# Kernel tuning notes

Hardware: AMD Instinct MI355X
Metric: run time of the kernel (lower is better)

The kernel has to match this reference:

```python
import jax, jax.numpy as jnp
import numpy as np

B, N, DIM, H = 8, 1024, 768, 12
D = DIM // H
SCALE = D ** -0.5
EPS = 1e-5


def setup_inputs() -> dict:
    key = jax.random.key(0)
    ks = jax.random.split(key, 6)
    s = 0.02
    return {
        "x": jax.random.normal(ks[0], (B, N, DIM), jnp.float32),
        "w_qv": jax.random.normal(ks[1], (2 * DIM, DIM), jnp.float32) * s,
        "ext_k": jax.random.normal(ks[2], (1, H, N, D), jnp.float32),
        "ext_bias": jax.random.normal(ks[3], (1, H, N, N), jnp.float32),
        "bn_gamma": jnp.ones((H,), jnp.float32),
        "bn_beta": jnp.zeros((H,), jnp.float32),
        "w_proj": jax.random.normal(ks[4], (DIM, DIM), jnp.float32) * s,
        "b_proj": jnp.zeros((DIM,), jnp.float32),
    }


def reference(x, w_qv, ext_k, ext_bias, bn_gamma, bn_beta, w_proj, b_proj):
    b, n, c = x.shape
    # qv projection (no bias), split into q and v
    qv = jnp.einsum('bnc,ec->bne', x, w_qv)  # [B,N,2C]
    q, v = jnp.split(qv, 2, axis=-1)
    # b n (h d) -> b h n d
    q = q.reshape(b, n, H, D).transpose(0, 2, 1, 3)
    v = v.reshape(b, n, H, D).transpose(0, 2, 1, 3)
    # scores: (q @ ext_k^T + bias) * scale  -> [B,H,N,N]
    attn = (jnp.einsum('bhnd,xhmd->bhnm', q, ext_k) + ext_bias) * SCALE
    # BatchNorm2d over heads (training-mode batch stats over B,N,N)
    mean = jnp.mean(attn, axis=(0, 2, 3), keepdims=True)
    var = jnp.mean(jnp.square(attn - mean), axis=(0, 2, 3), keepdims=True)
    attn = (attn - mean) * jax.lax.rsqrt(var + EPS)
    attn = attn * bn_gamma[None, :, None, None] + bn_beta[None, :, None, None]
    # softmax over keys, dropout p=0
    attn = jax.nn.softmax(attn, axis=-1)
    out = jnp.einsum('bhnm,bhmd->bhnd', attn, v)
    out = out.transpose(0, 2, 1, 3).reshape(b, n, c)  # b h n d -> b n (h d)
    return jnp.einsum('bnc,oc->bno', out, w_proj) + b_proj
```

## Files before the change

kernel.cpp:

```cpp
#include <hip/hip_runtime.h>
#include <cstdint>

#define B_    8
#define N_    1024
#define DIM_  768
#define H_    12
#define D_    64
#define SCALE_ 0.125f
#define GQ_   32
#define GK_   4

typedef unsigned short u16;
typedef short bf16x8 __attribute__((ext_vector_type(8)));
typedef float f32x4  __attribute__((ext_vector_type(4)));

__device__ __forceinline__ u16 f2b(float f) {
  union { float f; unsigned u; } v; v.f = f;
  unsigned r = v.u + 0x7FFFu + ((v.u >> 16) & 1u);
  return (u16)(r >> 16);
}
__device__ __forceinline__ float b2f(u16 h) {
  union { unsigned u; float f; } v; v.u = ((unsigned)h) << 16; return v.f;
}
__device__ __forceinline__ void gl2lds16(const void* g, void* l) {
  __builtin_amdgcn_global_load_lds(
      (const __attribute__((address_space(1))) void*)g,
      (__attribute__((address_space(3))) void*)l, 16, 0, 0);
}

__global__ __launch_bounds__(256) void cast_all(
    const float4* __restrict__ s0, u16* __restrict__ d0, int n0,
    const float4* __restrict__ s1, u16* __restrict__ d1, int n1,
    const float4* __restrict__ s2, u16* __restrict__ d2, int n2,
    const float4* __restrict__ s3, u16* __restrict__ d3, int n3)
{
  int i = blockIdx.x * 256 + threadIdx.x;
  const float4* s; u16* d; int off;
  if (i < n0)               { s = s0; d = d0; off = i; }
  else if (i < n0+n1)       { s = s1; d = d1; off = i - n0; }
  else if (i < n0+n1+n2)    { s = s2; d = d2; off = i - n0 - n1; }
  else if (i < n0+n1+n2+n3) { s = s3; d = d3; off = i - n0 - n1 - n2; }
  else return;
  float4 v = s[off];
  ushort4 o; o.x = f2b(v.x); o.y = f2b(v.y); o.z = f2b(v.z); o.w = f2b(v.w);
  *(ushort4*)(d + (size_t)off * 4) = o;
}

__global__ __launch_bounds__(256) void qv_gemm(
    const u16* __restrict__ A, const u16* __restrict__ W,
    u16* __restrict__ qo, u16* __restrict__ vo)
{
  __shared__ u16 As[128*32];
  __shared__ u16 Bs[128*32];
  const int tid = threadIdx.x, lane = tid & 63, wid = tid >> 6;
  const int m0 = blockIdx.y * 128, n0 = blockIdx.x * 128;
  const int wm = (wid >> 1) * 64, wn = (wid & 1) * 64;
  const int lr = lane & 15, lq = lane >> 4;
  f32x4 acc[4][4] = {};
  for (int k0 = 0; k0 < 768; k0 += 32) {
#pragma unroll
    for (int it = 0; it < 2; ++it) {
      int c = it * 256 + tid;
      int row = c >> 2, c8 = c & 3;
      gl2lds16(A + (size_t)(m0 + row) * 768 + k0 + c8 * 8, (char*)As + (it*256 + wid*64) * 16);
      gl2lds16(W + (size_t)(n0 + row) * 768 + k0 + c8 * 8, (char*)Bs + (it*256 + wid*64) * 16);
    }
    __syncthreads();
    bf16x8 af[4], bfr[4];
#pragma unroll
    for (int i = 0; i < 4; ++i) {
      af[i]  = *(const bf16x8*)&As[(wm + i*16 + lr) * 32 + lq * 8];
      bfr[i] = *(const bf16x8*)&Bs[(wn + i*16 + lr) * 32 + lq * 8];
    }
#pragma unroll
    for (int mi = 0; mi < 4; ++mi)
#pragma unroll
      for (int nj = 0; nj < 4; ++nj)
        acc[mi][nj] = __builtin_amdgcn_mfma_f32_16x16x32_bf16(af[mi], bfr[nj], acc[mi][nj], 0, 0, 0);
    __syncthreads();
  }
#pragma unroll
  for (int mi = 0; mi < 4; ++mi)
#pragma unroll
    for (int nj = 0; nj < 4; ++nj)
#pragma unroll
      for (int r = 0; r < 4; ++r) {
        int row = m0 + wm + mi*16 + lq*4 + r;
        int col = n0 + wn + nj*16 + lr;
        u16 bv = f2b(acc[mi][nj][r]);
        int b = row >> 10, n = row & 1023;
        if (col < 768) { int h = col >> 6, d = col & 63;
          qo[(((size_t)(b*12 + h)) << 16) + (n << 6) + d] = bv;
        } else { int e = col - 768; int h = e >> 6, d = e & 63;
          vo[(((size_t)(b*12 + h)) << 16) + (n << 6) + d] = bv;
        }
      }
}

__global__ __launch_bounds__(256) void transpose_v(
    const u16* __restrict__ v, u16* __restrict__ vt,
    const u16* __restrict__ kk, u16* __restrict__ ktT)
{
  __shared__ u16 t[64][65];
  int y = blockIdx.y, n0 = blockIdx.x * 64, tid = threadIdx.x;
  const u16* src; u16* dst;
  if (y < 96) { src = v  + (((size_t)y) << 16) + (size_t)n0 * 64;      dst = vt  + (((size_t)y) << 16) + n0; }
  else { int h = y - 96; src = kk + (((size_t)h) << 16) + (size_t)n0 * 64; dst = ktT + (((size_t)h) << 16) + n0; }
#pragma unroll
  for (int i = 0; i < 16; ++i) {
    int e = i*256 + tid; t[e >> 6][e & 63] = src[e];
  }
  __syncthreads();
#pragma unroll
  for (int i = 0; i < 16; ++i) {
    int e = i*256 + tid; int d = e >> 6, r = e & 63;
    dst[(size_t)d * 1024 + r] = t[r][d];
  }
}

__global__ __launch_bounds__(256) void qs_kernel(const u16* __restrict__ q, float* __restrict__ qs)
{
  int idx = blockIdx.x * 256 + threadIdx.x;
  int h = idx >> 16, rem = idx & 65535;
  float s = 0.f;
#pragma unroll
  for (int b = 0; b < 8; ++b) s += b2f(q[(((size_t)(b*12 + h)) << 16) + rem]);
  qs[idx] = s;
}

__global__ __launch_bounds__(256) void gram_kernel(
    const u16* __restrict__ src, float* __restrict__ gpart,
    int rows_per_block, int b_interleaved)
{
  __shared__ float t[64*68];
  const int h = blockIdx.y, r0 = blockIdx.x * rows_per_block, tid = threadIdx.x;
  const int rr = (tid >> 4) * 4;
  const int cc = (tid & 15) * 4;
  float a[4][4] = {{0.f}};
  for (int t0 = 0; t0 < rows_per_block; t0 += 64) {
#pragma unroll
    for (int i = 0; i < 4; ++i) {
      int e = i*256 + tid;
      int r = e >> 4, d4 = (e & 15) * 4;
      int gr = r0 + t0 + r;
      size_t addr;
      if (b_interleaved) { int b = gr >> 10, n = gr & 1023;
        addr = (((size_t)(b*12 + h)) << 16) + (n << 6) + d4; }
      else addr = (((size_t)h) << 16) + ((size_t)gr << 6) + d4;
      ushort4 u = *(const ushort4*)(src + addr);
      float4 f; f.x = b2f(u.x); f.y = b2f(u.y); f.z = b2f(u.z); f.w = b2f(u.w);
      *(float4*)&t[r*68 + d4] = f;
    }
    __syncthreads();
#pragma unroll 4
    for (int m = 0; m < 64; ++m) {
      float4 rv = *(const float4*)&t[m*68 + rr];
      float4 cv = *(const float4*)&t[m*68 + cc];
      a[0][0] += rv.x*cv.x; a[0][1] += rv.x*cv.y; a[0][2] += rv.x*cv.z; a[0][3] += rv.x*cv.w;
      a[1][0] += rv.y*cv.x; a[1][1] += rv.y*cv.y; a[1][2] += rv.y*cv.z; a[1][3] += rv.y*cv.w;
      a[2][0] += rv.z*cv.x; a[2][1] += rv.z*cv.y; a[2][2] += rv.z*cv.z; a[2][3] += rv.z*cv.w;
      a[3][0] += rv.w*cv.x; a[3][1] += rv.w*cv.y; a[3][2] += rv.w*cv.z; a[3][3] += rv.w*cv.w;
    }
    __syncthreads();
  }
  float* g = gpart + (((size_t)blockIdx.x) * 12 + h) * 4096;
#pragma unroll
  for (int i = 0; i < 4; ++i)
    *(float4*)&g[(rr + i)*64 + cc] = make_float4(a[i][0], a[i][1], a[i][2], a[i][3]);
}

__global__ __launch_bounds__(256) void bias_stats(
    const float* __restrict__ bias, const u16* __restrict__ ktT,
    const float* __restrict__ qs, float* __restrict__ acc)
{
  __shared__ float red[12];
  const int tid = threadIdx.x, lane = tid & 63, wid = tid >> 6;
  const int lr = lane & 15, lq = lane >> 4;
  const int h = blockIdx.y;
  const int nb = blockIdx.x & 15, mb = blockIdx.x >> 4;
  const int n0 = nb * 64 + wid * 16;
  const size_t brow = (((size_t)h) << 20) + ((size_t)(n0 + lr) << 10);
  const size_t kbase = ((size_t)h) << 16;
  f32x4 kb[4] = {};
  float sb = 0.f, sb2 = 0.f;
#pragma unroll
  for (int ms = 0; ms < 4; ++ms) {
    const int m0 = mb * 256 + ms * 64;
#pragma unroll
    for (int ks = 0; ks < 2; ++ks) {
      const int mc = m0 + ks * 32 + lq * 8;
      float4 b0 = *(const float4*)(bias + brow + mc);
      float4 b1 = *(const float4*)(bias + brow + mc + 4);
      sb  += b0.x + b0.y + b0.z + b0.w + b1.x + b1.y + b1.z + b1.w;
      sb2 += b0.x*b0.x + b0.y*b0.y + b0.z*b0.z + b0.w*b0.w
           + b1.x*b1.x + b1.y*b1.y + b1.z*b1.z + b1.w*b1.w;
      union { bf16x8 v; u16 u[8]; } af;
      af.u[0] = f2b(b0.x); af.u[1] = f2b(b0.y); af.u[2] = f2b(b0.z); af.u[3] = f2b(b0.w);
      af.u[4] = f2b(b1.x); af.u[5] = f2b(b1.y); af.u[6] = f2b(b1.z); af.u[7] = f2b(b1.w);
#pragma unroll
      for (int dj = 0; dj < 4; ++dj) {
        bf16x8 bfr = *(const bf16x8*)(ktT + kbase + (size_t)(dj*16 + lr) * 1024 + mc);
        kb[dj] = __builtin_amdgcn_mfma_f32_16x16x32_bf16(af.v, bfr, kb[dj], 0, 0, 0);
      }
    }
  }
  float cross = 0.f;
#pragma unroll
  for (int dj = 0; dj < 4; ++dj)
#pragma unroll
    for (int r = 0; r < 4; ++r)
      cross += kb[dj][r] *
               qs[kbase + ((size_t)(nb*64 + wid*16 + lq*4 + r) << 6) + dj*16 + lr];
#pragma unroll
  for (int s = 32; s; s >>= 1) {
    sb += __shfl_xor(sb, s); sb2 += __shfl_xor(sb2, s); cross += __shfl_xor(cross, s);
  }
  if (lane == 0) { red[wid] = sb; red[4 + wid] = sb2; red[8 + wid] = cross; }
  __syncthreads();
  if (tid == 0) {
    atomicAdd(acc + h,      red[0] + red[1] + red[2] + red[3]);
    atomicAdd(acc + 12 + h, red[4] + red[5] + red[6] + red[7]);
    atomicAdd(acc + 24 + h, red[8] + red[9] + red[10] + red[11]);
  }
}

__global__ __launch_bounds__(256) void sums_kernel(
    const float* __restrict__ qs, const u16* __restrict__ kb16,
    float* __restrict__ qsum, float* __restrict__ ksum)
{
  __shared__ float red[256];
  int h = blockIdx.x, yc = blockIdx.y;
  int tid = threadIdx.x, d = tid & 63, qq = tid >> 6;
  if (yc < 8) {
    float s = 0.f;
    int nbase = yc * 128 + qq * 32;
    for (int n = 0; n < 32; ++n)
      s += qs[(((size_t)h) << 16) + ((size_t)(nbase + n) << 6) + d];
    red[tid] = s; __syncthreads();
    if (qq == 0) atomicAdd(&qsum[h*64 + d], red[d] + red[64+d] + red[128+d] + red[192+d]);
  } else {
    float s = 0.f;
    int nbase = qq * 256;
    for (int n = 0; n < 256; ++n)
      s += b2f(kb16[(((size_t)h) << 16) + ((size_t)(nbase + n) << 6) + d]);
    red[tid] = s; __syncthreads();
    if (qq == 0) ksum[h*64 + d] = red[d] + red[64+d] + red[128+d] + red[192+d];
  }
}

__global__ __launch_bounds__(256) void finalize_kernel(
    const float* __restrict__ qsum, const float* __restrict__ ksum,
    const float* __restrict__ Qgp, const float* __restrict__ Kgp,
    const float* __restrict__ acc, const float* __restrict__ gamma,
    float* __restrict__ temp)
{
  __shared__ float qg[4096];
  __shared__ float kg[4096];
  __shared__ float red[8];
  int h = blockIdx.x, tid = threadIdx.x, wid = tid >> 6, lane = tid & 63;
#pragma unroll
  for (int i = 0; i < 16; ++i) {
    int e = i*256 + tid;
    float q = 0.f, k = 0.f;
    for (int g = 0; g < GQ_; ++g) q += Qgp[(((size_t)g)*12 + h)*4096 + e];
#pragma unroll
    for (int g = 0; g < GK_; ++g) k += Kgp[(((size_t)g)*12 + h)*4096 + e];
    qg[e] = q; kg[e] = k;
  }
  __syncthreads();
  float s2 = 0.f;
#pragma unroll
  for (int i = 0; i < 16; ++i) { int e = i*256 + tid; s2 += qg[e]*kg[e]; }
  float s1 = (tid < 64) ? qsum[h*64 + tid] * ksum[h*64 + tid] : 0.f;
#pragma unroll
  for (int s = 32; s; s >>= 1) { s2 += __shfl_xor(s2, s); s1 += __shfl_xor(s1, s); }
  if (lane == 0) { red[wid] = s2; red[4 + wid] = s1; }
  __syncthreads();
  if (tid == 0) {
    double S2 = (double)red[0] + red[1] + red[2] + red[3];
    double S1 = (double)red[4];
    double M = 8388608.0;
    double Sb = acc[h], Sb2 = acc[12 + h], Cross = acc[24 + h];
    double Eraw  = (S1 + 8.0 * Sb) / M;
    double Eraw2 = (S2 + 2.0 * Cross + 8.0 * Sb2) / M;
    double var = (double)SCALE_ * (double)SCALE_ * (Eraw2 - Eraw * Eraw);
    double rstd = 1.0 / sqrt(var + 1e-5);
    temp[h] = (float)((double)gamma[h] * (double)SCALE_ * rstd);
  }
}

__global__ __launch_bounds__(256) void attn_kernel(
    const u16* __restrict__ q, const u16* __restrict__ k, const u16* __restrict__ vT,
    const float* __restrict__ bias, const float* __restrict__ temp, u16* __restrict__ out)
{
  __shared__ u16 qt[4096];
  __shared__ u16 kt[4096];
  __shared__ u16 vt[5120];
  __shared__ u16 pt[64*72];
  const int tid = threadIdx.x, lane = tid & 63, wid = tid >> 6;
  const int lr = lane & 15, lq = lane >> 4;
  const int X = blockIdx.x;
  const int g = X >> 6, r_ = X & 63, b = r_ >> 3, q8 = r_ & 7;
  const int p = g*8 + q8;
  const int h = p % 12, n0 = (p / 12) * 64;
  const size_t qbase = ((((size_t)b) * 12 + h) << 16) + ((size_t)n0 << 6);
  const size_t kbase = ((size_t)h) << 16;
  const size_t vbase = ((((size_t)b) * 12 + h) << 16);
  const size_t bbase = (((size_t)h) << 20) + ((size_t)n0 << 10);
  const float tmp = temp[h];
  const int rowl = wid*16 + lq*4;

#pragma unroll
  for (int it = 0; it < 2; ++it) {
    int c = it*256 + tid; int ks = c >> 8, r = (c >> 2) & 63, c8 = c & 3;
    gl2lds16(q + qbase + (size_t)r * 64 + ks*32 + c8*8, (char*)qt + (it*256 + wid*64) * 16);
  }
  for (int i = tid; i < 1024; i += 256) {
    int ks = i >> 9, rr = (i >> 5) & 15, cc = i & 31;
    vt[ks*2560 + (64 + rr)*32 + cc] = (rr == 0) ? (u16)0x3F80 : (u16)0;
  }
  f32x4 oacc[5] = {};

  for (int m0 = 0; m0 < 1024; m0 += 64) {
#pragma unroll
    for (int it = 0; it < 2; ++it) {
      int c = it*256 + tid; int ks = c >> 8, r = (c >> 2) & 63, c8 = c & 3;
      gl2lds16(k  + kbase + (size_t)(m0 + r) * 64 + ks*32 + c8*8, (char*)kt + (it*256 + wid*64) * 16);
      gl2lds16(vT + vbase + (size_t)r * 1024 + m0 + ks*32 + c8*8, (char*)vt + it*5120 + wid*1024);
    }
    float breg[4][4];
#pragma unroll
    for (int r = 0; r < 4; ++r)
#pragma unroll
      for (int nj = 0; nj < 4; ++nj)
        breg[r][nj] = bias[bbase + (size_t)(rowl + r) * 1024 + m0 + nj*16 + lr];
    __syncthreads();
    f32x4 s[4] = {};
#pragma unroll
    for (int ks = 0; ks < 2; ++ks) {
      bf16x8 aq = *(const bf16x8*)&qt[ks*2048 + (wid*16 + lr)*32 + lq*8];
#pragma unroll
      for (int nj = 0; nj < 4; ++nj) {
        bf16x8 bk = *(const bf16x8*)&kt[ks*2048 + (nj*16 + lr)*32 + lq*8];
        s[nj] = __builtin_amdgcn_mfma_f32_16x16x32_bf16(aq, bk, s[nj], 0, 0, 0);
      }
    }
#pragma unroll
    for (int r = 0; r < 4; ++r)
#pragma unroll
      for (int nj = 0; nj < 4; ++nj) {
        float pv = __expf((s[nj][r] + breg[r][nj]) * tmp);
        pt[(rowl + r)*72 + nj*16 + lr] = f2b(pv);
      }
#pragma unroll
    for (int ks = 0; ks < 2; ++ks) {
      bf16x8 ap = *(const bf16x8*)&pt[(wid*16 + lr)*72 + ks*32 + lq*8];
#pragma unroll
      for (int dj = 0; dj < 5; ++dj) {
        bf16x8 bv = *(const bf16x8*)&vt[ks*2560 + (dj*16 + lr)*32 + lq*8];
        oacc[dj] = __builtin_amdgcn_mfma_f32_16x16x32_bf16(ap, bv, oacc[dj], 0, 0, 0);
      }
    }
    __syncthreads();
  }
#pragma unroll
  for (int r = 0; r < 4; ++r) {
    float l = __shfl(oacc[4][r], lane & 48);
    float linv = 1.f / l;
    int n = n0 + rowl + r;
#pragma unroll
    for (int dj = 0; dj < 4; ++dj) {
      int col = h*64 + dj*16 + lr;
      out[((size_t)(b*1024 + n)) * 768 + col] = f2b(oacc[dj][r] * linv);
    }
  }
}

__global__ __launch_bounds__(256) void proj_gemm(
    const u16* __restrict__ A, const u16* __restrict__ W,
    const float* __restrict__ bp, float* __restrict__ out)
{
  __shared__ u16 As[128*32];
  __shared__ u16 Bs[128*32];
  const int tid = threadIdx.x, lane = tid & 63, wid = tid >> 6;
  const int m0 = blockIdx.y * 128, n0 = blockIdx.x * 128;
  const int wm = (wid >> 1) * 64, wn = (wid & 1) * 64;
  const int lr = lane & 15, lq = lane >> 4;
  f32x4 acc[4][4] = {};
  for (int k0 = 0; k0 < 768; k0 += 32) {
#pragma unroll
    for (int it = 0; it < 2; ++it) {
      int c = it*256 + tid; int row = c >> 2, c8 = c & 3;
      gl2lds16(A + (size_t)(m0 + row) * 768 + k0 + c8*8, (char*)As + (it*256 + wid*64) * 16);
      gl2lds16(W + (size_t)(n0 + row) * 768 + k0 + c8*8, (char*)Bs + (it*256 + wid*64) * 16);
    }
    __syncthreads();
    bf16x8 af[4], bfr[4];
#pragma unroll
    for (int i = 0; i < 4; ++i) {
      af[i]  = *(const bf16x8*)&As[(wm + i*16 + lr)*32 + lq*8];
      bfr[i] = *(const bf16x8*)&Bs[(wn + i*16 + lr)*32 + lq*8];
    }
#pragma unroll
    for (int mi = 0; mi < 4; ++mi)
#pragma unroll
      for (int nj = 0; nj < 4; ++nj)
        acc[mi][nj] = __builtin_amdgcn_mfma_f32_16x16x32_bf16(af[mi], bfr[nj], acc[mi][nj], 0, 0, 0);
    __syncthreads();
  }
#pragma unroll
  for (int mi = 0; mi < 4; ++mi)
#pragma unroll
    for (int nj = 0; nj < 4; ++nj)
#pragma unroll
      for (int r = 0; r < 4; ++r) {
        int row = m0 + wm + mi*16 + lq*4 + r;
        int col = n0 + wn + nj*16 + lr;
        out[(size_t)row * 768 + col] = acc[mi][nj][r] + bp[col];
      }
}

extern "C" void kernel_launch(void* const* d_in, const int* in_sizes, int n_in,
                              void* d_out, int out_size, void* d_ws, size_t ws_size,
                              hipStream_t stream)
{
  const float* x     = (const float*)d_in[0];
  const float* wqv   = (const float*)d_in[1];
  const float* ek    = (const float*)d_in[2];
  const float* ebias = (const float*)d_in[3];
  const float* gamma = (const float*)d_in[4];
  const float* wp    = (const float*)d_in[6];
  const float* bp    = (const float*)d_in[7];
  float* out = (float*)d_out;

  char* ws = (char*)d_ws;
  size_t off = 0;
  auto alloc = [&](size_t bytes) { char* p = ws + off; off += (bytes + 255) & ~(size_t)255; return p; };
  u16* x16   = (u16*)alloc((size_t)8192*768*2);
  u16* wqv16 = (u16*)alloc((size_t)1536*768*2);
  u16* wp16  = (u16*)alloc((size_t)768*768*2);
  u16* k16   = (u16*)alloc((size_t)12*1024*64*2);
  u16* ktT16 = (u16*)alloc((size_t)12*64*1024*2);
  u16* q16   = (u16*)alloc((size_t)8*12*1024*64*2);
  u16* v16   = (u16*)alloc((size_t)8*12*1024*64*2);
  u16* vt16  = (u16*)alloc((size_t)8*12*1024*64*2);
  float* qs  = (float*)alloc((size_t)12*1024*64*4);
  float* acc = (float*)alloc(3*12*4);
  float* qsum = (float*)alloc(12*64*4);
  float* ksum = (float*)alloc(12*64*4);
  size_t zbytes = (size_t)(((char*)ksum + 12*64*4) - (char*)acc);
  float* temp = (float*)alloc(12*4);
  float* Qgp = (float*)x16;
  float* Kgp = Qgp + (size_t)GQ_*12*4096;
  u16* attn16 = x16;

  hipMemsetAsync(acc, 0, zbytes, stream);

  {
    int c0 = 8192*768/4, c1 = 1536*768/4, c2 = 768*768/4, c3 = 12*1024*64/4;
    int total = c0 + c1 + c2 + c3;
    cast_all<<<(total + 255)/256, 256, 0, stream>>>(
        (const float4*)x, x16, c0, (const float4*)wqv, wqv16, c1,
        (const float4*)wp, wp16, c2, (const float4*)ek, k16, c3);
  }
  qv_gemm<<<dim3(12, 64), 256, 0, stream>>>(x16, wqv16, q16, v16);
  transpose_v<<<dim3(16, 108), 256, 0, stream>>>(v16, vt16, k16, ktT16);
  qs_kernel<<<3072, 256, 0, stream>>>(q16, qs);
  gram_kernel<<<dim3(GK_, 12), 256, 0, stream>>>(k16, Kgp, 1024/GK_, 0);
  gram_kernel<<<dim3(GQ_, 12), 256, 0, stream>>>(q16, Qgp, 8192/GQ_, 1);
  bias_stats<<<dim3(64, 12), 256, 0, stream>>>(ebias, ktT16, qs, acc);
  sums_kernel<<<dim3(12, 9), 256, 0, stream>>>(qs, k16, qsum, ksum);
  finalize_kernel<<<12, 256, 0, stream>>>(qsum, ksum, Qgp, Kgp, acc, gamma, temp);
  attn_kernel<<<dim3(1536), 256, 0, stream>>>(q16, k16, vt16, ebias, temp, attn16);
  proj_gemm<<<dim3(6, 64), 256, 0, stream>>>(attn16, wp16, bp, out);
}
```

Baseline: 323.1 us.

## Prefetch bias tiles, use exp2, swizzle P in LDS, transpose PV MFMA

After: 323.3 us. About the same (+0.1%).

```diff
diff --git a/kernel.cpp b/kernel.cpp
--- a/kernel.cpp
+++ b/kernel.cpp
@@ -19,9 +19,18 @@
   unsigned r = v.u + 0x7FFFu + ((v.u >> 16) & 1u);
   return (u16)(r >> 16);
 }
+__device__ __forceinline__ u16 phu(float f) {
+  union { float f; unsigned u; } v; v.f = f;
+  return (u16)((v.u + 0x8000u) >> 16);
+}
 __device__ __forceinline__ float b2f(u16 h) {
   union { unsigned u; float f; } v; v.u = ((unsigned)h) << 16; return v.f;
 }
+#if __has_builtin(__builtin_amdgcn_exp2f)
+__device__ __forceinline__ float exp2fast(float x) { return __builtin_amdgcn_exp2f(x); }
+#else
+__device__ __forceinline__ float exp2fast(float x) { return __expf(x * 0.69314718f); }
+#endif
 __device__ __forceinline__ void gl2lds16(const void* g, void* l) {
   __builtin_amdgcn_global_load_lds(
       (const __attribute__((address_space(1))) void*)g,
@@ -296,7 +305,7 @@
   __shared__ u16 qt[4096];
   __shared__ u16 kt[4096];
   __shared__ u16 vt[5120];
-  __shared__ u16 pt[64*72];
+  __shared__ u16 pt[4608];
   const int tid = threadIdx.x, lane = tid & 63, wid = tid >> 6;
   const int lr = lane & 15, lq = lane >> 4;
   const int X = blockIdx.x;
@@ -307,8 +316,12 @@
   const size_t kbase = ((size_t)h) << 16;
   const size_t vbase = ((((size_t)b) * 12 + h) << 16);
   const size_t bbase = (((size_t)h) << 20) + ((size_t)n0 << 10);
-  const float tmp = temp[h];
+  const float tmp2 = temp[h] * 1.44269504f;
   const int rowl = wid*16 + lq*4;
+  const float* brow0 = bias + bbase + (size_t)(rowl+0) * 1024 + lr;
+  const float* brow1 = brow0 + 1024;
+  const float* brow2 = brow1 + 1024;
+  const float* brow3 = brow2 + 1024;
 
 #pragma unroll
   for (int it = 0; it < 2; ++it) {
@@ -320,6 +333,12 @@
     vt[ks*2560 + (64 + rr)*32 + cc] = (rr == 0) ? (u16)0x3F80 : (u16)0;
   }
   f32x4 oacc[5] = {};
+  float bn[4][4];
+#pragma unroll
+  for (int nj = 0; nj < 4; ++nj) {
+    bn[0][nj] = brow0[nj*16]; bn[1][nj] = brow1[nj*16];
+    bn[2][nj] = brow2[nj*16]; bn[3][nj] = brow3[nj*16];
+  }
 
   for (int m0 = 0; m0 < 1024; m0 += 64) {
 #pragma unroll
@@ -328,14 +347,26 @@
       gl2lds16(k  + kbase + (size_t)(m0 + r) * 64 + ks*32 + c8*8, (char*)kt + (it*256 + wid*64) * 16);
       gl2lds16(vT + vbase + (size_t)r * 1024 + m0 + ks*32 + c8*8, (char*)vt + it*5120 + wid*1024);
     }
-    float breg[4][4];
+    float bc[4][4];
 #pragma unroll
     for (int r = 0; r < 4; ++r)
 #pragma unroll
-      for (int nj = 0; nj < 4; ++nj)
-        breg[r][nj] = bias[bbase + (size_t)(rowl + r) * 1024 + m0 + nj*16 + lr];
-    __syncthreads();
-    f32x4 s[4] = {};
+      for (int nj = 0; nj < 4; ++nj) bc[r][nj] = bn[r][nj];
+    if (m0 < 960) {
+      int mo = m0 + 64;
+#pragma unroll
+      for (int nj = 0; nj < 4; ++nj) {
+        bn[0][nj] = brow0[mo + nj*16]; bn[1][nj] = brow1[mo + nj*16];
+        bn[2][nj] = brow2[mo + nj*16]; bn[3][nj] = brow3[mo + nj*16];
+      }
+    }
+    __syncthreads();
+    f32x4 s[4];
+#pragma unroll
+    for (int nj = 0; nj < 4; ++nj) {
+      s[nj][0] = bc[0][nj]; s[nj][1] = bc[1][nj];
+      s[nj][2] = bc[2][nj]; s[nj][3] = bc[3][nj];
+    }
 #pragma unroll
     for (int ks = 0; ks < 2; ++ks) {
       bf16x8 aq = *(const bf16x8*)&qt[ks*2048 + (wid*16 + lr)*32 + lq*8];
@@ -349,30 +380,31 @@
     for (int r = 0; r < 4; ++r)
 #pragma unroll
       for (int nj = 0; nj < 4; ++nj) {
-        float pv = __expf((s[nj][r] + breg[r][nj]) * tmp);
-        pt[(rowl + r)*72 + nj*16 + lr] = f2b(pv);
+        float pv = exp2fast(s[nj][r] * tmp2);
+        int sw = ((nj*2 + (lr >> 3)) ^ lq) * 8 + (lr & 7);
+        pt[(rowl + r)*72 + sw] = phu(pv);
       }
 #pragma unroll
     for (int ks = 0; ks < 2; ++ks) {
-      bf16x8 ap = *(const bf16x8*)&pt[(wid*16 + lr)*72 + ks*32 + lq*8];
+      bf16x8 bp = *(const bf16x8*)&pt[(wid*16 + lr)*72 + (((ks*4 + lq) ^ (lr >> 2)) * 8)];
 #pragma unroll
       for (int dj = 0; dj < 5; ++dj) {
-        bf16x8 bv = *(const bf16x8*)&vt[ks*2560 + (dj*16 + lr)*32 + lq*8];
-        oacc[dj] = __builtin_amdgcn_mfma_f32_16x16x32_bf16(ap, bv, oacc[dj], 0, 0, 0);
-      }
-    }
-    __syncthreads();
-  }
-#pragma unroll
-  for (int r = 0; r < 4; ++r) {
-    float l = __shfl(oacc[4][r], lane & 48);
-    float linv = 1.f / l;
-    int n = n0 + rowl + r;
-#pragma unroll
-    for (int dj = 0; dj < 4; ++dj) {
-      int col = h*64 + dj*16 + lr;
-      out[((size_t)(b*1024 + n)) * 768 + col] = f2b(oacc[dj][r] * linv);
-    }
+        bf16x8 av = *(const bf16x8*)&vt[ks*2560 + (dj*16 + lr)*32 + lq*8];
+        oacc[dj] = __builtin_amdgcn_mfma_f32_16x16x32_bf16(av, bp, oacc[dj], 0, 0, 0);
+      }
+    }
+    __syncthreads();
+  }
+  float l = __shfl(oacc[4][0], lr);
+  float linv = __builtin_amdgcn_rcpf(l);
+  int n = n0 + wid*16 + lr;
+  u16* orow = out + (size_t)(b*1024 + n) * 768 + h*64 + lq*4;
+#pragma unroll
+  for (int dj = 0; dj < 4; ++dj) {
+    ushort4 o;
+    o.x = f2b(oacc[dj][0] * linv); o.y = f2b(oacc[dj][1] * linv);
+    o.z = f2b(oacc[dj][2] * linv); o.w = f2b(oacc[dj][3] * linv);
+    *(ushort4*)(orow + dj*16) = o;
   }
 }
 
```

## Double query rows per attention block and keep Q fragments in registers

Applied to the files above, without the earlier changes.

Measured after the change: 310.6 us. 1.04x faster.

```diff
diff --git a/kernel.cpp b/kernel.cpp
--- a/kernel.cpp
+++ b/kernel.cpp
@@ -19,9 +19,18 @@
   unsigned r = v.u + 0x7FFFu + ((v.u >> 16) & 1u);
   return (u16)(r >> 16);
 }
+__device__ __forceinline__ u16 phu(float f) {
+  union { float f; unsigned u; } v; v.f = f;
+  return (u16)((v.u + 0x8000u) >> 16);
+}
 __device__ __forceinline__ float b2f(u16 h) {
   union { unsigned u; float f; } v; v.u = ((unsigned)h) << 16; return v.f;
 }
+#if __has_builtin(__builtin_amdgcn_exp2f)
+__device__ __forceinline__ float exp2fast(float x) { return __builtin_amdgcn_exp2f(x); }
+#else
+__device__ __forceinline__ float exp2fast(float x) { return __expf(x * 0.69314718f); }
+#endif
 __device__ __forceinline__ void gl2lds16(const void* g, void* l) {
   __builtin_amdgcn_global_load_lds(
       (const __attribute__((address_space(1))) void*)g,
@@ -293,33 +302,42 @@
     const u16* __restrict__ q, const u16* __restrict__ k, const u16* __restrict__ vT,
     const float* __restrict__ bias, const float* __restrict__ temp, u16* __restrict__ out)
 {
-  __shared__ u16 qt[4096];
   __shared__ u16 kt[4096];
   __shared__ u16 vt[5120];
-  __shared__ u16 pt[64*72];
+  __shared__ u16 pt[128*72];
   const int tid = threadIdx.x, lane = tid & 63, wid = tid >> 6;
   const int lr = lane & 15, lq = lane >> 4;
   const int X = blockIdx.x;
   const int g = X >> 6, r_ = X & 63, b = r_ >> 3, q8 = r_ & 7;
   const int p = g*8 + q8;
-  const int h = p % 12, n0 = (p / 12) * 64;
+  const int h = p % 12, n0 = (p / 12) * 128;
   const size_t qbase = ((((size_t)b) * 12 + h) << 16) + ((size_t)n0 << 6);
   const size_t kbase = ((size_t)h) << 16;
   const size_t vbase = ((((size_t)b) * 12 + h) << 16);
   const size_t bbase = (((size_t)h) << 20) + ((size_t)n0 << 10);
-  const float tmp = temp[h];
-  const int rowl = wid*16 + lq*4;
-
-#pragma unroll
-  for (int it = 0; it < 2; ++it) {
-    int c = it*256 + tid; int ks = c >> 8, r = (c >> 2) & 63, c8 = c & 3;
-    gl2lds16(q + qbase + (size_t)r * 64 + ks*32 + c8*8, (char*)qt + (it*256 + wid*64) * 16);
-  }
+  const float tmp2 = temp[h] * 1.44269504f;
+  const int W = wid * 32;
+
+  bf16x8 aq[2][2];
+#pragma unroll
+  for (int mi = 0; mi < 2; ++mi)
+#pragma unroll
+    for (int ks = 0; ks < 2; ++ks)
+      aq[mi][ks] = *(const bf16x8*)(q + qbase + (size_t)(W + mi*16 + lr)*64 + ks*32 + lq*8);
+
   for (int i = tid; i < 1024; i += 256) {
     int ks = i >> 9, rr = (i >> 5) & 15, cc = i & 31;
     vt[ks*2560 + (64 + rr)*32 + cc] = (rr == 0) ? (u16)0x3F80 : (u16)0;
   }
-  f32x4 oacc[5] = {};
+
+  const float* br[2][4];
+#pragma unroll
+  for (int mi = 0; mi < 2; ++mi)
+#pragma unroll
+    for (int r = 0; r < 4; ++r)
+      br[mi][r] = bias + bbase + (size_t)(W + mi*16 + lq*4 + r) * 1024 + lr;
+
+  f32x4 oacc[5][2] = {};
 
   for (int m0 = 0; m0 < 1024; m0 += 64) {
 #pragma unroll
@@ -328,50 +346,62 @@
       gl2lds16(k  + kbase + (size_t)(m0 + r) * 64 + ks*32 + c8*8, (char*)kt + (it*256 + wid*64) * 16);
       gl2lds16(vT + vbase + (size_t)r * 1024 + m0 + ks*32 + c8*8, (char*)vt + it*5120 + wid*1024);
     }
-    float breg[4][4];
-#pragma unroll
-    for (int r = 0; r < 4; ++r)
+    f32x4 s[2][4];
+#pragma unroll
+    for (int mi = 0; mi < 2; ++mi)
 #pragma unroll
       for (int nj = 0; nj < 4; ++nj)
-        breg[r][nj] = bias[bbase + (size_t)(rowl + r) * 1024 + m0 + nj*16 + lr];
-    __syncthreads();
-    f32x4 s[4] = {};
+#pragma unroll
+        for (int r = 0; r < 4; ++r)
+          s[mi][nj][r] = br[mi][r][m0 + nj*16];
+    __syncthreads();
 #pragma unroll
     for (int ks = 0; ks < 2; ++ks) {
-      bf16x8 aq = *(const bf16x8*)&qt[ks*2048 + (wid*16 + lr)*32 + lq*8];
 #pragma unroll
       for (int nj = 0; nj < 4; ++nj) {
         bf16x8 bk = *(const bf16x8*)&kt[ks*2048 + (nj*16 + lr)*32 + lq*8];
-        s[nj] = __builtin_amdgcn_mfma_f32_16x16x32_bf16(aq, bk, s[nj], 0, 0, 0);
+#pragma unroll
+        for (int mi = 0; mi < 2; ++mi)
+          s[mi][nj] = __builtin_amdgcn_mfma_f32_16x16x32_bf16(aq[mi][ks], bk, s[mi][nj], 0, 0, 0);
       }
     }
 #pragma unroll
-    for (int r = 0; r < 4; ++r)
-#pragma unroll
-      for (int nj = 0; nj < 4; ++nj) {
-        float pv = __expf((s[nj][r] + breg[r][nj]) * tmp);
-        pt[(rowl + r)*72 + nj*16 + lr] = f2b(pv);
+    for (int mi = 0; mi < 2; ++mi)
+#pragma unroll
+      for (int r = 0; r < 4; ++r) {
+        int row = W + mi*16 + lq*4 + r;
+#pragma unroll
+        for (int nj = 0; nj < 4; ++nj)
+          pt[row*72 + nj*16 + lr] = phu(exp2fast(s[mi][nj][r] * tmp2));
       }
 #pragma unroll
     for (int ks = 0; ks < 2; ++ks) {
-      bf16x8 ap = *(const bf16x8*)&pt[(wid*16 + lr)*72 + ks*32 + lq*8];
+      bf16x8 bp[2];
+#pragma unroll
+      for (int ni = 0; ni < 2; ++ni)
+        bp[ni] = *(const bf16x8*)&pt[(W + ni*16 + lr)*72 + ks*32 + lq*8];
 #pragma unroll
       for (int dj = 0; dj < 5; ++dj) {
-        bf16x8 bv = *(const bf16x8*)&vt[ks*2560 + (dj*16 + lr)*32 + lq*8];
-        oacc[dj] = __builtin_amdgcn_mfma_f32_16x16x32_bf16(ap, bv, oacc[dj], 0, 0, 0);
+        bf16x8 av = *(const bf16x8*)&vt[ks*2560 + (dj*16 + lr)*32 + lq*8];
+#pragma unroll
+        for (int ni = 0; ni < 2; ++ni)
+          oacc[dj][ni] = __builtin_amdgcn_mfma_f32_16x16x32_bf16(av, bp[ni], oacc[dj][ni], 0, 0, 0);
       }
     }
     __syncthreads();
   }
 #pragma unroll
-  for (int r = 0; r < 4; ++r) {
-    float l = __shfl(oacc[4][r], lane & 48);
-    float linv = 1.f / l;
-    int n = n0 + rowl + r;
+  for (int ni = 0; ni < 2; ++ni) {
+    float l = __shfl(oacc[4][ni][0], lr);
+    float linv = __builtin_amdgcn_rcpf(l);
+    int n = n0 + W + ni*16 + lr;
+    u16* orow = out + (size_t)(b*1024 + n) * 768 + h*64 + lq*4;
 #pragma unroll
     for (int dj = 0; dj < 4; ++dj) {
-      int col = h*64 + dj*16 + lr;
-      out[((size_t)(b*1024 + n)) * 768 + col] = f2b(oacc[dj][r] * linv);
+      ushort4 o;
+      o.x = f2b(oacc[dj][ni][0] * linv); o.y = f2b(oacc[dj][ni][1] * linv);
+      o.z = f2b(oacc[dj][ni][2] * linv); o.w = f2b(oacc[dj][ni][3] * linv);
+      *(ushort4*)(orow + dj*16) = o;
     }
   }
 }
@@ -471,6 +501,6 @@
   bias_stats<<<dim3(64, 12), 256, 0, stream>>>(ebias, ktT16, qs, acc);
   sums_kernel<<<dim3(12, 9), 256, 0, stream>>>(qs, k16, qsum, ksum);
   finalize_kernel<<<12, 256, 0, stream>>>(qsum, ksum, Qgp, Kgp, acc, gamma, temp);
-  attn_kernel<<<dim3(1536), 256, 0, stream>>>(q16, k16, vt16, ebias, temp, attn16);
+  attn_kernel<<<dim3(768), 256, 0, stream>>>(q16, k16, vt16, ebias, temp, attn16);
   proj_gemm<<<dim3(6, 64), 256, 0, stream>>>(attn16, wp16, bp, out);
 }
```
